# Kernel tuning notes

Measured on AMD Instinct MI355X. Metric: run time of the kernel, lower is better.

The kernel has to match this reference:

```python
import jax, jax.numpy as jnp
from jax import lax
import numpy as np

B, L, V, E, F, K, Y = 8, 2048, 51919, 100, 256, 9, 8921
PAD = K // 2  # 4, so conv output length == L


def setup_inputs() -> dict:
    key = jax.random.key(0)
    ks = jax.random.split(key, 8)
    return {
        "x": jax.random.randint(ks[0], (B, L), 0, 51917, dtype=jnp.int32),
        "target": jax.random.uniform(ks[1], (B, Y), dtype=jnp.float32),
        "embed_W": jax.random.normal(ks[2], (V, E), dtype=jnp.float32) * 0.1,
        "conv_w": jax.random.normal(ks[3], (F, E, K), dtype=jnp.float32) * (1.0 / np.sqrt(E * K)),
        "conv_b": jax.random.normal(ks[4], (F,), dtype=jnp.float32) * 0.01,
        "U_w": jax.random.normal(ks[5], (Y, F), dtype=jnp.float32) * (1.0 / np.sqrt(F)),
        "final_w": jax.random.normal(ks[6], (Y, F), dtype=jnp.float32) * (1.0 / np.sqrt(F)),
        "final_b": jax.random.normal(ks[7], (Y,), dtype=jnp.float32) * 0.01,
    }


def reference(x, target, embed_W, conv_w, conv_b, U_w, final_w, final_b):
    # Embedding lookup (dropout is identity at eval time)
    h = embed_W[x]                         # [B, L, E]
    h = jnp.transpose(h, (0, 2, 1))        # [B, E, L]
    # Conv1d, same-length padding
    h = lax.conv_general_dilated(
        h, conv_w, window_strides=(1,), padding=[(PAD, PAD)],
        dimension_numbers=("NCH", "OIH", "NCH"))
    h = jnp.tanh(h + conv_b[None, :, None])  # [B, F, L]
    h = jnp.transpose(h, (0, 2, 1))          # [B, L, F]
    # Per-label attention: scores [B, Y, L]
    scores = jnp.einsum("yf,blf->byl", U_w, h)
    alpha = jax.nn.softmax(scores, axis=2)   # [B, Y, L]
    m = jnp.einsum("byl,blf->byf", alpha, h)  # [B, Y, F]
    yhat = jnp.sum(final_w[None, :, :] * m, axis=2) + final_b  # [B, Y]
    # BCE with logits, mean reduction (stable form)
    loss = jnp.mean(jnp.maximum(yhat, 0.0) - yhat * target
                    + jnp.log1p(jnp.exp(-jnp.abs(yhat))))
    return yhat, loss, alpha
```

## Files before the change

kernel.cpp:

```cpp
#include <hip/hip_runtime.h>
#include <hip/hip_bf16.h>
#include <math.h>

#define B_ 8
#define L_ 2048
#define E_ 100
#define F_ 256
#define KW 9
#define Y_ 8921
#define YP 8960
#define KC 928
#define MC 16384

#define VMCNT(n) asm volatile("s_waitcnt vmcnt(" #n ")" ::: "memory")
#define CFENCE() asm volatile("" ::: "memory")

typedef __bf16 bf16x8 __attribute__((ext_vector_type(8)));
typedef float f32x4 __attribute__((ext_vector_type(4)));

__device__ __forceinline__ unsigned short f2bf(float v) {
  __hip_bfloat16 h = __float2bfloat16(v);
  return *reinterpret_cast<unsigned short*>(&h);
}

__device__ __forceinline__ void gld_lds16(const unsigned short* g, unsigned short* l) {
  __builtin_amdgcn_global_load_lds((const __attribute__((address_space(1))) void*)g,
                                   (__attribute__((address_space(3))) void*)l,
                                   16, 0, 0);
}

template <int STRIDE>
__device__ __forceinline__ void stage_tile(const unsigned short* __restrict__ g,
                                           unsigned short* __restrict__ lds, int tid) {
#pragma unroll
  for (int r = 0; r < 2; ++r) {
    int c = r * 256 + tid;
    gld_lds16(g + (size_t)(c >> 2) * STRIDE + (c & 3) * 8, lds + c * 8);
  }
}

__global__ __launch_bounds__(256) void im2col_kernel(const int* __restrict__ x,
                                                     const float* __restrict__ embedW,
                                                     unsigned short* __restrict__ im) {
  int idx = blockIdx.x * 256 + threadIdx.x;
  if (idx >= MC * (KC / 4)) return;
  int row = idx / (KC / 4), g4 = idx - row * (KC / 4);
  int kk = g4 * 4;
  ushort4 o = {0, 0, 0, 0};
  if (kk < 900) {
    int k = kk / 100, e = kk - k * 100;
    int b = row >> 11, l = row & 2047;
    int ls = l + k - 4;
    if (ls >= 0 && ls < L_) {
      const float4 v = *reinterpret_cast<const float4*>(
          &embedW[(size_t)x[b * L_ + ls] * E_ + e]);
      o.x = f2bf(v.x); o.y = f2bf(v.y); o.z = f2bf(v.z); o.w = f2bf(v.w);
    }
  }
  *reinterpret_cast<ushort4*>(&im[(size_t)idx * 4]) = o;
}

__global__ __launch_bounds__(256) void wpack_kernel(const float* __restrict__ convw,
                                                    unsigned short* __restrict__ wc) {
  int idx = blockIdx.x * 256 + threadIdx.x;
  if (idx >= F_ * KC) return;
  int f = idx / KC, kk = idx - f * KC;
  float v = 0.f;
  if (kk < 900) {
    int k = kk / 100, e = kk - k * 100;
    v = convw[f * 900 + e * 9 + k];
  }
  wc[idx] = f2bf(v);
}

__global__ __launch_bounds__(256) void ufpack_kernel(const float* __restrict__ Uw,
                                                     const float* __restrict__ Fww,
                                                     unsigned short* __restrict__ Ub,
                                                     unsigned short* __restrict__ Fwb) {
  int idx = blockIdx.x * 256 + threadIdx.x;
  if (idx >= 2 * YP * F_) return;
  int sel = idx / (YP * F_);
  int r = idx - sel * (YP * F_);
  int y = r / F_, f = r - y * F_;
  float v = (y < Y_) ? (sel ? Fww[y * F_ + f] : Uw[y * F_ + f]) : 0.f;
  (sel ? Fwb : Ub)[r] = f2bf(v);
}

__global__ __launch_bounds__(256) void conv_gemm(const unsigned short* __restrict__ A,
                                                 const unsigned short* __restrict__ Bt,
                                                 const float* __restrict__ convb,
                                                 unsigned short* __restrict__ hb) {
  __shared__ unsigned short As[3][128 * 32], Bs[3][128 * 32];
  const int mt = blockIdx.x, nt = blockIdx.y, tid = threadIdx.x;
  const unsigned short* Ag = A + (size_t)mt * 128 * KC;
  const unsigned short* Bg = Bt + (size_t)nt * 128 * KC;
  f32x4 acc[4][4] = {};
  const int lane = tid & 63, wv = tid >> 6;
  const int wy = wv >> 1, wx = wv & 1, lr = lane & 15, lq = lane >> 4;
  stage_tile<KC>(Ag, As[0], tid);
  stage_tile<KC>(Bg, Bs[0], tid);
  for (int kt = 0; kt < 29; ++kt) {
    const int cur = kt % 3;
    if (kt + 1 < 29) {
      const int nxt = (kt + 1) % 3;
      stage_tile<KC>(Ag + (kt + 1) * 32, As[nxt], tid);
      stage_tile<KC>(Bg + (kt + 1) * 32, Bs[nxt], tid);
      VMCNT(4);
    } else {
      VMCNT(0);
    }
    __builtin_amdgcn_s_barrier();
    CFENCE();
    bf16x8 a[4], bb[4];
#pragma unroll
    for (int i = 0; i < 4; ++i) a[i] = *(const bf16x8*)&As[cur][(wy * 64 + i * 16 + lr) * 32 + lq * 8];
#pragma unroll
    for (int j = 0; j < 4; ++j) bb[j] = *(const bf16x8*)&Bs[cur][(wx * 64 + j * 16 + lr) * 32 + lq * 8];
#pragma unroll
    for (int i = 0; i < 4; ++i)
#pragma unroll
      for (int j = 0; j < 4; ++j)
        acc[i][j] = __builtin_amdgcn_mfma_f32_16x16x32_bf16(a[i], bb[j], acc[i][j], 0, 0, 0);
  }
#pragma unroll
  for (int j = 0; j < 4; ++j) {
    const int n = nt * 128 + wx * 64 + j * 16 + lr;
    const float cb = convb[n];
#pragma unroll
    for (int i = 0; i < 4; ++i)
#pragma unroll
      for (int r = 0; r < 4; ++r) {
        const int m = mt * 128 + wy * 64 + i * 16 + lq * 4 + r;
        hb[(size_t)m * F_ + n] = f2bf(tanhf(acc[i][j][r] + cb));
      }
  }
}

__global__ __launch_bounds__(256) void scores_sum(const unsigned short* __restrict__ U,
                                                  const unsigned short* __restrict__ hb,
                                                  float* __restrict__ Spart) {
  __shared__ unsigned short As[3][128 * 32], Bs[3][128 * 32];
  __shared__ float rsum[128][2];
  const int yt = blockIdx.x, lt = blockIdx.y, b = blockIdx.z, tid = threadIdx.x;
  const unsigned short* Ag = U + (size_t)yt * 128 * F_;
  const unsigned short* Bg = hb + ((size_t)b * L_ + lt * 128) * F_;
  f32x4 acc[4][4] = {};
  const int lane = tid & 63, wv = tid >> 6;
  const int wy = wv >> 1, wx = wv & 1, lr = lane & 15, lq = lane >> 4;
  stage_tile<F_>(Ag, As[0], tid);
  stage_tile<F_>(Bg, Bs[0], tid);
  for (int kt = 0; kt < 8; ++kt) {
    const int cur = kt % 3;
    if (kt + 1 < 8) {
      const int nxt = (kt + 1) % 3;
      stage_tile<F_>(Ag + (kt + 1) * 32, As[nxt], tid);
      stage_tile<F_>(Bg + (kt + 1) * 32, Bs[nxt], tid);
      VMCNT(4);
    } else {
      VMCNT(0);
    }
    __builtin_amdgcn_s_barrier();
    CFENCE();
    bf16x8 a[4], bb[4];
#pragma unroll
    for (int i = 0; i < 4; ++i) a[i] = *(const bf16x8*)&As[cur][(wy * 64 + i * 16 + lr) * 32 + lq * 8];
#pragma unroll
    for (int j = 0; j < 4; ++j) bb[j] = *(const bf16x8*)&Bs[cur][(wx * 64 + j * 16 + lr) * 32 + lq * 8];
#pragma unroll
    for (int i = 0; i < 4; ++i)
#pragma unroll
      for (int j = 0; j < 4; ++j)
        acc[i][j] = __builtin_amdgcn_mfma_f32_16x16x32_bf16(a[i], bb[j], acc[i][j], 0, 0, 0);
  }
#pragma unroll
  for (int i = 0; i < 4; ++i)
#pragma unroll
    for (int r = 0; r < 4; ++r) {
      float rs = 0.f;
#pragma unroll
      for (int j = 0; j < 4; ++j) rs += __expf(acc[i][j][r]);
#pragma unroll
      for (int off = 1; off < 16; off <<= 1) rs += __shfl_xor(rs, off);
      if (lr == 0) rsum[wy * 64 + i * 16 + lq * 4 + r][wx] = rs;
    }
  __syncthreads();
  if (tid < 128)
    Spart[((size_t)b * YP + yt * 128 + tid) * 16 + lt] = rsum[tid][0] + rsum[tid][1];
}

__global__ __launch_bounds__(256) void sinv_kernel(const float* __restrict__ Spart,
                                                   float* __restrict__ Sinv) {
  int idx = blockIdx.x * 256 + threadIdx.x;
  if (idx >= B_ * YP) return;
  float s = 0.f;
#pragma unroll
  for (int t = 0; t < 16; ++t) s += Spart[(size_t)idx * 16 + t];
  Sinv[idx] = 1.f / s;
}

__global__ __launch_bounds__(256) void dual_gemm(const unsigned short* __restrict__ U,
                                                 const unsigned short* __restrict__ Fw,
                                                 const unsigned short* __restrict__ hb,
                                                 const float* __restrict__ Sinv,
                                                 float* __restrict__ alpha,
                                                 float* __restrict__ Npart) {
  __shared__ unsigned short As[3][128 * 32], As2[3][128 * 32], Bs[3][128 * 32];
  __shared__ float rsum[128][2];
  __shared__ float sinv[128];
  const int yt = blockIdx.x, lt = blockIdx.y, b = blockIdx.z, tid = threadIdx.x;
  if (tid < 128) sinv[tid] = Sinv[b * YP + yt * 128 + tid];
  __syncthreads();
  const unsigned short* Ag = U + (size_t)yt * 128 * F_;
  const unsigned short* Ag2 = Fw + (size_t)yt * 128 * F_;
  const unsigned short* Bg = hb + ((size_t)b * L_ + lt * 128) * F_;
  f32x4 accs[4][4] = {}, accg[4][4] = {};
  const int lane = tid & 63, wv = tid >> 6;
  const int wy = wv >> 1, wx = wv & 1, lr = lane & 15, lq = lane >> 4;
  stage_tile<F_>(Ag, As[0], tid);
  stage_tile<F_>(Ag2, As2[0], tid);
  stage_tile<F_>(Bg, Bs[0], tid);
  for (int kt = 0; kt < 8; ++kt) {
    const int cur = kt % 3;
    if (kt + 1 < 8) {
      const int nxt = (kt + 1) % 3;
      stage_tile<F_>(Ag + (kt + 1) * 32, As[nxt], tid);
      stage_tile<F_>(Ag2 + (kt + 1) * 32, As2[nxt], tid);
      stage_tile<F_>(Bg + (kt + 1) * 32, Bs[nxt], tid);
      VMCNT(6);
    } else {
      VMCNT(0);
    }
    __builtin_amdgcn_s_barrier();
    CFENCE();
    bf16x8 a1[4], a2[4], bb[4];
#pragma unroll
    for (int i = 0; i < 4; ++i) {
      a1[i] = *(const bf16x8*)&As[cur][(wy * 64 + i * 16 + lr) * 32 + lq * 8];
      a2[i] = *(const bf16x8*)&As2[cur][(wy * 64 + i * 16 + lr) * 32 + lq * 8];
    }
#pragma unroll
    for (int j = 0; j < 4; ++j) bb[j] = *(const bf16x8*)&Bs[cur][(wx * 64 + j * 16 + lr) * 32 + lq * 8];
#pragma unroll
    for (int i = 0; i < 4; ++i)
#pragma unroll
      for (int j = 0; j < 4; ++j) {
        accs[i][j] = __builtin_amdgcn_mfma_f32_16x16x32_bf16(a1[i], bb[j], accs[i][j], 0, 0, 0);
        accg[i][j] = __builtin_amdgcn_mfma_f32_16x16x32_bf16(a2[i], bb[j], accg[i][j], 0, 0, 0);
      }
  }
#pragma unroll
  for (int i = 0; i < 4; ++i)
#pragma unroll
    for (int r = 0; r < 4; ++r) {
      const int ml = wy * 64 + i * 16 + lq * 4 + r;
      const int y = yt * 128 + ml;
      const float si = sinv[ml];
      float ns = 0.f;
#pragma unroll
      for (int j = 0; j < 4; ++j) {
        const float av = __expf(accs[i][j][r]) * si;
        ns += av * accg[i][j][r];
        if (y < Y_) {
          const int l = lt * 128 + wx * 64 + j * 16 + lr;
          alpha[((size_t)b * Y_ + y) * L_ + l] = av;
        }
      }
#pragma unroll
      for (int off = 1; off < 16; off <<= 1) ns += __shfl_xor(ns, off);
      if (lr == 0) rsum[ml][wx] = ns;
    }
  __syncthreads();
  if (tid < 128)
    Npart[((size_t)b * YP + yt * 128 + tid) * 16 + lt] = rsum[tid][0] + rsum[tid][1];
}

__global__ __launch_bounds__(256) void yhat_loss_kernel(const float* __restrict__ Npart,
                                                        const float* __restrict__ Fb,
                                                        const float* __restrict__ target,
                                                        float* __restrict__ yhat,
                                                        float* __restrict__ part) {
  __shared__ float red[256];
  float s = 0.f;
  for (int i = blockIdx.x * 256 + threadIdx.x; i < B_ * Y_; i += gridDim.x * 256) {
    int b = i / Y_, y = i - b * Y_;
    float yh = Fb[y];
#pragma unroll
    for (int t = 0; t < 16; ++t) yh += Npart[((size_t)b * YP + y) * 16 + t];
    yhat[i] = yh;
    float tg = target[i];
    s += fmaxf(yh, 0.f) - yh * tg + log1pf(expf(-fabsf(yh)));
  }
  red[threadIdx.x] = s;
  __syncthreads();
  for (int o = 128; o > 0; o >>= 1) {
    if (threadIdx.x < o) red[threadIdx.x] += red[threadIdx.x + o];
    __syncthreads();
  }
  if (threadIdx.x == 0) part[blockIdx.x] = red[0];
}

__global__ __launch_bounds__(128) void loss_final_kernel(const float* __restrict__ part,
                                                         float* __restrict__ loss) {
  __shared__ float red[128];
  red[threadIdx.x] = part[threadIdx.x];
  __syncthreads();
  for (int o = 64; o > 0; o >>= 1) {
    if (threadIdx.x < o) red[threadIdx.x] += red[threadIdx.x + o];
    __syncthreads();
  }
  if (threadIdx.x == 0) loss[0] = red[0] * (1.f / (float)(B_ * Y_));
}

extern "C" void kernel_launch(void* const* d_in, const int* in_sizes, int n_in,
                              void* d_out, int out_size, void* d_ws, size_t ws_size,
                              hipStream_t stream) {
  const int* x = (const int*)d_in[0];
  const float* target = (const float*)d_in[1];
  const float* embedW = (const float*)d_in[2];
  const float* convw = (const float*)d_in[3];
  const float* convb = (const float*)d_in[4];
  const float* Uw = (const float*)d_in[5];
  const float* Fww = (const float*)d_in[6];
  const float* Fb = (const float*)d_in[7];

  float* out = (float*)d_out;
  float* yhat = out;
  float* loss = out + 71368;
  float* alpha = out + 71369;

  char* w = (char*)d_ws;
  size_t off = 0;
  auto alloc = [&](size_t bytes) -> void* {
    void* p = w + off;
    off += (bytes + 255) & ~(size_t)255;
    return p;
  };
  unsigned short* im2col = (unsigned short*)alloc((size_t)MC * KC * 2);
  unsigned short* wconv = (unsigned short*)alloc((size_t)F_ * KC * 2);
  unsigned short* Ub = (unsigned short*)alloc((size_t)YP * F_ * 2);
  unsigned short* Fwb = (unsigned short*)alloc((size_t)YP * F_ * 2);
  unsigned short* hb = (unsigned short*)alloc((size_t)MC * F_ * 2);
  float* Spart = (float*)alloc((size_t)B_ * YP * 16 * 4);
  float* Sinv = (float*)alloc((size_t)B_ * YP * 4);
  float* Npart = (float*)alloc((size_t)B_ * YP * 16 * 4);
  float* lpart = (float*)alloc(128 * 4);

  im2col_kernel<<<(MC * (KC / 4) + 255) / 256, 256, 0, stream>>>(x, embedW, im2col);
  wpack_kernel<<<(F_ * KC + 255) / 256, 256, 0, stream>>>(convw, wconv);
  ufpack_kernel<<<(2 * YP * F_ + 255) / 256, 256, 0, stream>>>(Uw, Fww, Ub, Fwb);
  conv_gemm<<<dim3(128, 2), 256, 0, stream>>>(im2col, wconv, convb, hb);
  scores_sum<<<dim3(70, 16, 8), 256, 0, stream>>>(Ub, hb, Spart);
  sinv_kernel<<<(B_ * YP + 255) / 256, 256, 0, stream>>>(Spart, Sinv);
  dual_gemm<<<dim3(70, 16, 8), 256, 0, stream>>>(Ub, Fwb, hb, Sinv, alpha, Npart);
  yhat_loss_kernel<<<128, 256, 0, stream>>>(Npart, Fb, target, yhat, lpart);
  loss_final_kernel<<<1, 128, 0, stream>>>(lpart, loss);
}
```

Measured before the change: 1.002 ms.

## Fuse attention score, softmax, and weighted sum into one persistent per-label-tile kernel

Replaces the scores_sum, sinv, dual_gemm and yhat reduction kernels with a single attn_fused kernel. Each block keeps a 128-label tile of U and final_w resident in LDS and loops over the full sequence twice: once to accumulate softmax denominators, once to write alpha and accumulate the yhat dot product. It also adds an XOR swizzle to LDS staging in conv_gemm to reduce bank conflicts. This removes the partial-sum buffers and extra launches, but the grid shrinks to 560 blocks of 512 threads with large LDS per block, which lowers parallelism and occupancy.

```diff
diff --git a/kernel.cpp b/kernel.cpp
--- a/kernel.cpp
+++ b/kernel.cpp
@@ -29,13 +29,14 @@
                                    16, 0, 0);
 }
 
-template <int STRIDE>
+template <int STRIDE, int NT>
 __device__ __forceinline__ void stage_tile(const unsigned short* __restrict__ g,
                                            unsigned short* __restrict__ lds, int tid) {
 #pragma unroll
-  for (int r = 0; r < 2; ++r) {
-    int c = r * 256 + tid;
-    gld_lds16(g + (size_t)(c >> 2) * STRIDE + (c & 3) * 8, lds + c * 8);
+  for (int r = 0; r < 512 / NT; ++r) {
+    int c = r * NT + tid;
+    int row = c >> 2, s = c & 3;
+    gld_lds16(g + (size_t)row * STRIDE + ((s ^ ((row >> 1) & 3)) * 8), lds + c * 8);
   }
 }
 
@@ -97,14 +98,15 @@
   f32x4 acc[4][4] = {};
   const int lane = tid & 63, wv = tid >> 6;
   const int wy = wv >> 1, wx = wv & 1, lr = lane & 15, lq = lane >> 4;
-  stage_tile<KC>(Ag, As[0], tid);
-  stage_tile<KC>(Bg, Bs[0], tid);
+  const int bOff = (lq ^ ((lr >> 1) & 3)) * 8;
+  stage_tile<KC, 256>(Ag, As[0], tid);
+  stage_tile<KC, 256>(Bg, Bs[0], tid);
   for (int kt = 0; kt < 29; ++kt) {
     const int cur = kt % 3;
     if (kt + 1 < 29) {
       const int nxt = (kt + 1) % 3;
-      stage_tile<KC>(Ag + (kt + 1) * 32, As[nxt], tid);
-      stage_tile<KC>(Bg + (kt + 1) * 32, Bs[nxt], tid);
+      stage_tile<KC, 256>(Ag + (kt + 1) * 32, As[nxt], tid);
+      stage_tile<KC, 256>(Bg + (kt + 1) * 32, Bs[nxt], tid);
       VMCNT(4);
     } else {
       VMCNT(0);
@@ -113,9 +115,9 @@
     CFENCE();
     bf16x8 a[4], bb[4];
 #pragma unroll
-    for (int i = 0; i < 4; ++i) a[i] = *(const bf16x8*)&As[cur][(wy * 64 + i * 16 + lr) * 32 + lq * 8];
-#pragma unroll
-    for (int j = 0; j < 4; ++j) bb[j] = *(const bf16x8*)&Bs[cur][(wx * 64 + j * 16 + lr) * 32 + lq * 8];
+    for (int i = 0; i < 4; ++i) a[i] = *(const bf16x8*)&As[cur][(wy * 64 + i * 16 + lr) * 32 + bOff];
+#pragma unroll
+    for (int j = 0; j < 4; ++j) bb[j] = *(const bf16x8*)&Bs[cur][(wx * 64 + j * 16 + lr) * 32 + bOff];
 #pragma unroll
     for (int i = 0; i < 4; ++i)
 #pragma unroll
@@ -136,159 +138,206 @@
   }
 }
 
-__global__ __launch_bounds__(256) void scores_sum(const unsigned short* __restrict__ U,
-                                                  const unsigned short* __restrict__ hb,
-                                                  float* __restrict__ Spart) {
-  __shared__ unsigned short As[3][128 * 32], Bs[3][128 * 32];
-  __shared__ float rsum[128][2];
-  const int yt = blockIdx.x, lt = blockIdx.y, b = blockIdx.z, tid = threadIdx.x;
-  const unsigned short* Ag = U + (size_t)yt * 128 * F_;
-  const unsigned short* Bg = hb + ((size_t)b * L_ + lt * 128) * F_;
-  f32x4 acc[4][4] = {};
+__global__ __launch_bounds__(512, 1) void attn_fused(const unsigned short* __restrict__ U,
+                                                     const unsigned short* __restrict__ Fw,
+                                                     const unsigned short* __restrict__ hb,
+                                                     const float* __restrict__ Fb,
+                                                     float* __restrict__ alpha,
+                                                     float* __restrict__ yhat) {
+  __shared__ unsigned short Us[128 * 256];
+  __shared__ unsigned short Fws[128 * 256];
+  __shared__ unsigned short Bs[3][128 * 32];
+  const int yt = blockIdx.x, b = blockIdx.y, tid = threadIdx.x;
   const int lane = tid & 63, wv = tid >> 6;
-  const int wy = wv >> 1, wx = wv & 1, lr = lane & 15, lq = lane >> 4;
-  stage_tile<F_>(Ag, As[0], tid);
-  stage_tile<F_>(Bg, Bs[0], tid);
-  for (int kt = 0; kt < 8; ++kt) {
-    const int cur = kt % 3;
-    if (kt + 1 < 8) {
-      const int nxt = (kt + 1) % 3;
-      stage_tile<F_>(Ag + (kt + 1) * 32, As[nxt], tid);
-      stage_tile<F_>(Bg + (kt + 1) * 32, Bs[nxt], tid);
-      VMCNT(4);
+  const int wy = wv >> 2, wx = wv & 3, lr = lane & 15, lq = lane >> 4;
+  const unsigned short* Ug = U + (size_t)yt * 128 * F_;
+  const unsigned short* Fg = Fw + (size_t)yt * 128 * F_;
+  const unsigned short* Hg = hb + (size_t)b * L_ * F_;
+
+#pragma unroll
+  for (int r = 0; r < 8; ++r) {
+    int c = r * 512 + tid;
+    int row = c >> 5, s = c & 31;
+    gld_lds16(Ug + row * F_ + ((s ^ (row & 7)) * 8), Us + c * 8);
+  }
+  {
+    int c = tid, row = c >> 2, s = c & 3;
+    gld_lds16(Hg + (size_t)row * F_ + ((s ^ ((row >> 1) & 3)) * 8), Bs[0] + c * 8);
+  }
+  VMCNT(0);
+  __builtin_amdgcn_s_barrier();
+  CFENCE();
+
+  const int bOff = (lq ^ ((lr >> 1) & 3)) * 8;
+  const int lr7 = lr & 7;
+
+  float rsA[4][4] = {};
+  f32x4 acc[4][2];
+  for (int t = 0; t < 128; ++t) {
+    const int kt = t & 7;
+    if (t + 1 < 128) {
+      const int c = tid, row = c >> 2, s = c & 3;
+      const int lt1 = (t + 1) >> 3, kt1 = (t + 1) & 7;
+      gld_lds16(Hg + (size_t)(lt1 * 128 + row) * F_ + kt1 * 32 + ((s ^ ((row >> 1) & 3)) * 8),
+                Bs[(t + 1) % 3] + c * 8);
+      VMCNT(1);
     } else {
       VMCNT(0);
     }
     __builtin_amdgcn_s_barrier();
     CFENCE();
-    bf16x8 a[4], bb[4];
-#pragma unroll
-    for (int i = 0; i < 4; ++i) a[i] = *(const bf16x8*)&As[cur][(wy * 64 + i * 16 + lr) * 32 + lq * 8];
-#pragma unroll
-    for (int j = 0; j < 4; ++j) bb[j] = *(const bf16x8*)&Bs[cur][(wx * 64 + j * 16 + lr) * 32 + lq * 8];
+    if (kt == 0) {
+#pragma unroll
+      for (int i = 0; i < 4; ++i)
+#pragma unroll
+        for (int j = 0; j < 2; ++j) acc[i][j] = (f32x4){0.f, 0.f, 0.f, 0.f};
+    }
+    const unsigned short* bs = Bs[t % 3];
+    const int colOff = (((kt * 4 + lq) ^ lr7)) * 8;
+    bf16x8 a[4], bbf[2];
+#pragma unroll
+    for (int i = 0; i < 4; ++i) a[i] = *(const bf16x8*)&Us[(wy * 64 + i * 16 + lr) * 256 + colOff];
+#pragma unroll
+    for (int j = 0; j < 2; ++j) bbf[j] = *(const bf16x8*)&bs[(wx * 32 + j * 16 + lr) * 32 + bOff];
 #pragma unroll
     for (int i = 0; i < 4; ++i)
 #pragma unroll
-      for (int j = 0; j < 4; ++j)
-        acc[i][j] = __builtin_amdgcn_mfma_f32_16x16x32_bf16(a[i], bb[j], acc[i][j], 0, 0, 0);
-  }
+      for (int j = 0; j < 2; ++j)
+        acc[i][j] = __builtin_amdgcn_mfma_f32_16x16x32_bf16(a[i], bbf[j], acc[i][j], 0, 0, 0);
+    if (kt == 7) {
+#pragma unroll
+      for (int i = 0; i < 4; ++i)
+#pragma unroll
+        for (int r = 0; r < 4; ++r) {
+          float rs = __expf(acc[i][0][r]) + __expf(acc[i][1][r]);
+#pragma unroll
+          for (int off = 1; off < 16; off <<= 1) rs += __shfl_xor(rs, off);
+          rsA[i][r] += rs;
+        }
+    }
+  }
+
+#pragma unroll
+  for (int r = 0; r < 8; ++r) {
+    int c = r * 512 + tid;
+    int row = c >> 5, s = c & 31;
+    gld_lds16(Fg + row * F_ + ((s ^ (row & 7)) * 8), Fws + c * 8);
+  }
+  __syncthreads();
+  float* red = (float*)Bs;
 #pragma unroll
   for (int i = 0; i < 4; ++i)
 #pragma unroll
+    for (int r = 0; r < 4; ++r)
+      if (lr == 0) red[(wy * 64 + i * 16 + lq * 4 + r) * 4 + wx] = rsA[i][r];
+  __syncthreads();
+  float si[4][4];
+#pragma unroll
+  for (int i = 0; i < 4; ++i)
+#pragma unroll
     for (int r = 0; r < 4; ++r) {
-      float rs = 0.f;
-#pragma unroll
-      for (int j = 0; j < 4; ++j) rs += __expf(acc[i][j][r]);
-#pragma unroll
-      for (int off = 1; off < 16; off <<= 1) rs += __shfl_xor(rs, off);
-      if (lr == 0) rsum[wy * 64 + i * 16 + lq * 4 + r][wx] = rs;
-    }
-  __syncthreads();
-  if (tid < 128)
-    Spart[((size_t)b * YP + yt * 128 + tid) * 16 + lt] = rsum[tid][0] + rsum[tid][1];
-}
-
-__global__ __launch_bounds__(256) void sinv_kernel(const float* __restrict__ Spart,
-                                                   float* __restrict__ Sinv) {
-  int idx = blockIdx.x * 256 + threadIdx.x;
-  if (idx >= B_ * YP) return;
-  float s = 0.f;
-#pragma unroll
-  for (int t = 0; t < 16; ++t) s += Spart[(size_t)idx * 16 + t];
-  Sinv[idx] = 1.f / s;
-}
-
-__global__ __launch_bounds__(256) void dual_gemm(const unsigned short* __restrict__ U,
-                                                 const unsigned short* __restrict__ Fw,
-                                                 const unsigned short* __restrict__ hb,
-                                                 const float* __restrict__ Sinv,
-                                                 float* __restrict__ alpha,
-                                                 float* __restrict__ Npart) {
-  __shared__ unsigned short As[3][128 * 32], As2[3][128 * 32], Bs[3][128 * 32];
-  __shared__ float rsum[128][2];
-  __shared__ float sinv[128];
-  const int yt = blockIdx.x, lt = blockIdx.y, b = blockIdx.z, tid = threadIdx.x;
-  if (tid < 128) sinv[tid] = Sinv[b * YP + yt * 128 + tid];
-  __syncthreads();
-  const unsigned short* Ag = U + (size_t)yt * 128 * F_;
-  const unsigned short* Ag2 = Fw + (size_t)yt * 128 * F_;
-  const unsigned short* Bg = hb + ((size_t)b * L_ + lt * 128) * F_;
-  f32x4 accs[4][4] = {}, accg[4][4] = {};
-  const int lane = tid & 63, wv = tid >> 6;
-  const int wy = wv >> 1, wx = wv & 1, lr = lane & 15, lq = lane >> 4;
-  stage_tile<F_>(Ag, As[0], tid);
-  stage_tile<F_>(Ag2, As2[0], tid);
-  stage_tile<F_>(Bg, Bs[0], tid);
-  for (int kt = 0; kt < 8; ++kt) {
-    const int cur = kt % 3;
-    if (kt + 1 < 8) {
-      const int nxt = (kt + 1) % 3;
-      stage_tile<F_>(Ag + (kt + 1) * 32, As[nxt], tid);
-      stage_tile<F_>(Ag2 + (kt + 1) * 32, As2[nxt], tid);
-      stage_tile<F_>(Bg + (kt + 1) * 32, Bs[nxt], tid);
-      VMCNT(6);
+      const int row = wy * 64 + i * 16 + lq * 4 + r;
+      si[i][r] = 1.f / (red[row * 4] + red[row * 4 + 1] + red[row * 4 + 2] + red[row * 4 + 3]);
+    }
+  __syncthreads();
+
+  {
+    int c = tid, row = c >> 2, s = c & 3;
+    gld_lds16(Hg + (size_t)row * F_ + ((s ^ ((row >> 1) & 3)) * 8), Bs[0] + c * 8);
+  }
+  VMCNT(0);
+  __builtin_amdgcn_s_barrier();
+  CFENCE();
+  float nsA[4][4] = {};
+  f32x4 accs[4][2], accg[4][2];
+  for (int t = 0; t < 128; ++t) {
+    const int kt = t & 7, lt = t >> 3;
+    if (t + 1 < 128) {
+      const int c = tid, row = c >> 2, s = c & 3;
+      const int lt1 = (t + 1) >> 3, kt1 = (t + 1) & 7;
+      gld_lds16(Hg + (size_t)(lt1 * 128 + row) * F_ + kt1 * 32 + ((s ^ ((row >> 1) & 3)) * 8),
+                Bs[(t + 1) % 3] + c * 8);
+      VMCNT(1);
     } else {
       VMCNT(0);
     }
     __builtin_amdgcn_s_barrier();
     CFENCE();
-    bf16x8 a1[4], a2[4], bb[4];
+    if (kt == 0) {
+#pragma unroll
+      for (int i = 0; i < 4; ++i)
+#pragma unroll
+        for (int j = 0; j < 2; ++j) {
+          accs[i][j] = (f32x4){0.f, 0.f, 0.f, 0.f};
+          accg[i][j] = (f32x4){0.f, 0.f, 0.f, 0.f};
+        }
+    }
+    const unsigned short* bs = Bs[t % 3];
+    const int colOff = (((kt * 4 + lq) ^ lr7)) * 8;
+    bf16x8 a1[4], a2[4], bbf[2];
 #pragma unroll
     for (int i = 0; i < 4; ++i) {
-      a1[i] = *(const bf16x8*)&As[cur][(wy * 64 + i * 16 + lr) * 32 + lq * 8];
-      a2[i] = *(const bf16x8*)&As2[cur][(wy * 64 + i * 16 + lr) * 32 + lq * 8];
-    }
-#pragma unroll
-    for (int j = 0; j < 4; ++j) bb[j] = *(const bf16x8*)&Bs[cur][(wx * 64 + j * 16 + lr) * 32 + lq * 8];
+      a1[i] = *(const bf16x8*)&Us[(wy * 64 + i * 16 + lr) * 256 + colOff];
+      a2[i] = *(const bf16x8*)&Fws[(wy * 64 + i * 16 + lr) * 256 + colOff];
+    }
+#pragma unroll
+    for (int j = 0; j < 2; ++j) bbf[j] = *(const bf16x8*)&bs[(wx * 32 + j * 16 + lr) * 32 + bOff];
 #pragma unroll
     for (int i = 0; i < 4; ++i)
 #pragma unroll
-      for (int j = 0; j < 4; ++j) {
-        accs[i][j] = __builtin_amdgcn_mfma_f32_16x16x32_bf16(a1[i], bb[j], accs[i][j], 0, 0, 0);
-        accg[i][j] = __builtin_amdgcn_mfma_f32_16x16x32_bf16(a2[i], bb[j], accg[i][j], 0, 0, 0);
+      for (int j = 0; j < 2; ++j) {
+        accs[i][j] = __builtin_amdgcn_mfma_f32_16x16x32_bf16(a1[i], bbf[j], accs[i][j], 0, 0, 0);
+        accg[i][j] = __builtin_amdgcn_mfma_f32_16x16x32_bf16(a2[i], bbf[j], accg[i][j], 0, 0, 0);
       }
-  }
+    if (kt == 7) {
+#pragma unroll
+      for (int i = 0; i < 4; ++i)
+#pragma unroll
+        for (int r = 0; r < 4; ++r) {
+          const int row = wy * 64 + i * 16 + lq * 4 + r;
+          const int y = yt * 128 + row;
+          const float sv = si[i][r];
+          float ns = 0.f;
+#pragma unroll
+          for (int j = 0; j < 2; ++j) {
+            const float av = __expf(accs[i][j][r]) * sv;
+            ns += av * accg[i][j][r];
+            if (y < Y_) {
+              const int l = lt * 128 + wx * 32 + j * 16 + lr;
+              alpha[((size_t)b * Y_ + y) * L_ + l] = av;
+            }
+          }
+#pragma unroll
+          for (int off = 1; off < 16; off <<= 1) ns += __shfl_xor(ns, off);
+          nsA[i][r] += ns;
+        }
+    }
+  }
+  __syncthreads();
+  float* red2 = (float*)Bs;
 #pragma unroll
   for (int i = 0; i < 4; ++i)
 #pragma unroll
-    for (int r = 0; r < 4; ++r) {
-      const int ml = wy * 64 + i * 16 + lq * 4 + r;
-      const int y = yt * 128 + ml;
-      const float si = sinv[ml];
-      float ns = 0.f;
-#pragma unroll
-      for (int j = 0; j < 4; ++j) {
-        const float av = __expf(accs[i][j][r]) * si;
-        ns += av * accg[i][j][r];
-        if (y < Y_) {
-          const int l = lt * 128 + wx * 64 + j * 16 + lr;
-          alpha[((size_t)b * Y_ + y) * L_ + l] = av;
-        }
-      }
-#pragma unroll
-      for (int off = 1; off < 16; off <<= 1) ns += __shfl_xor(ns, off);
-      if (lr == 0) rsum[ml][wx] = ns;
-    }
-  __syncthreads();
-  if (tid < 128)
-    Npart[((size_t)b * YP + yt * 128 + tid) * 16 + lt] = rsum[tid][0] + rsum[tid][1];
-}
-
-__global__ __launch_bounds__(256) void yhat_loss_kernel(const float* __restrict__ Npart,
-                                                        const float* __restrict__ Fb,
+    for (int r = 0; r < 4; ++r)
+      if (lr == 0) red2[(wy * 64 + i * 16 + lq * 4 + r) * 4 + wx] = nsA[i][r];
+  __syncthreads();
+  if (tid < 128) {
+    const int y = yt * 128 + tid;
+    if (y < Y_) {
+      yhat[(size_t)b * Y_ + y] = Fb[y] + red2[tid * 4] + red2[tid * 4 + 1] +
+                                 red2[tid * 4 + 2] + red2[tid * 4 + 3];
+    }
+  }
+}
+
+__global__ __launch_bounds__(256) void loss_part_kernel(const float* __restrict__ yhat,
                                                         const float* __restrict__ target,
-                                                        float* __restrict__ yhat,
                                                         float* __restrict__ part) {
   __shared__ float red[256];
   float s = 0.f;
   for (int i = blockIdx.x * 256 + threadIdx.x; i < B_ * Y_; i += gridDim.x * 256) {
-    int b = i / Y_, y = i - b * Y_;
-    float yh = Fb[y];
-#pragma unroll
-    for (int t = 0; t < 16; ++t) yh += Npart[((size_t)b * YP + y) * 16 + t];
-    yhat[i] = yh;
-    float tg = target[i];
-    s += fmaxf(yh, 0.f) - yh * tg + log1pf(expf(-fabsf(yh)));
+    float yh = yhat[i], t = target[i];
+    s += fmaxf(yh, 0.f) - yh * t + log1pf(expf(-fabsf(yh)));
   }
   red[threadIdx.x] = s;
   __syncthreads();
@@ -340,18 +389,13 @@
   unsigned short* Ub = (unsigned short*)alloc((size_t)YP * F_ * 2);
   unsigned short* Fwb = (unsigned short*)alloc((size_t)YP * F_ * 2);
   unsigned short* hb = (unsigned short*)alloc((size_t)MC * F_ * 2);
-  float* Spart = (float*)alloc((size_t)B_ * YP * 16 * 4);
-  float* Sinv = (float*)alloc((size_t)B_ * YP * 4);
-  float* Npart = (float*)alloc((size_t)B_ * YP * 16 * 4);
   float* lpart = (float*)alloc(128 * 4);
 
   im2col_kernel<<<(MC * (KC / 4) + 255) / 256, 256, 0, stream>>>(x, embedW, im2col);
   wpack_kernel<<<(F_ * KC + 255) / 256, 256, 0, stream>>>(convw, wconv);
   ufpack_kernel<<<(2 * YP * F_ + 255) / 256, 256, 0, stream>>>(Uw, Fww, Ub, Fwb);
   conv_gemm<<<dim3(128, 2), 256, 0, stream>>>(im2col, wconv, convb, hb);
-  scores_sum<<<dim3(70, 16, 8), 256, 0, stream>>>(Ub, hb, Spart);
-  sinv_kernel<<<(B_ * YP + 255) / 256, 256, 0, stream>>>(Spart, Sinv);
-  dual_gemm<<<dim3(70, 16, 8), 256, 0, stream>>>(Ub, Fwb, hb, Sinv, alpha, Npart);
-  yhat_loss_kernel<<<128, 256, 0, stream>>>(Npart, Fb, target, yhat, lpart);
+  attn_fused<<<dim3(70, 8), 512, 0, stream>>>(Ub, Fwb, hb, Fb, alpha, yhat);
+  loss_part_kernel<<<128, 256, 0, stream>>>(yhat, target, lpart);
   loss_final_kernel<<<1, 128, 0, stream>>>(lpart, loss);
 }
```

New measurement: 1.194 ms. 1.19x slower.

## Hold label weights in registers, swizzle LDS, and loop over L tiles in attention GEMMs

Applied to the files above, without the earlier changes.

Repacks U and final_w into an MFMA-fragment-friendly layout so each wave loads its A operands straight into registers once and keeps them there. The scores and dual GEMM kernels then iterate over several L tiles per block, streaming only h through LDS. Staging now uses an XOR-swizzled LDS layout in all GEMMs to cut bank conflicts. Npart partials drop from 16 to 8 per label. This removes repeated A-tile staging and the LDS traffic for A, at the cost of much higher register pressure (64 or 32 bf16x8 fragments per thread) and fewer blocks per launch.

```diff
diff --git a/kernel.cpp b/kernel.cpp
--- a/kernel.cpp
+++ b/kernel.cpp
@@ -6,13 +6,13 @@
 #define L_ 2048
 #define E_ 100
 #define F_ 256
-#define KW 9
 #define Y_ 8921
 #define YP 8960
 #define KC 928
 #define MC 16384
 
 #define VMCNT(n) asm volatile("s_waitcnt vmcnt(" #n ")" ::: "memory")
+#define LGKM0() asm volatile("s_waitcnt lgkmcnt(0)" ::: "memory")
 #define CFENCE() asm volatile("" ::: "memory")
 
 typedef __bf16 bf16x8 __attribute__((ext_vector_type(8)));
@@ -29,13 +29,14 @@
                                    16, 0, 0);
 }
 
-template <int STRIDE>
+template <int STRIDE, int NT>
 __device__ __forceinline__ void stage_tile(const unsigned short* __restrict__ g,
                                            unsigned short* __restrict__ lds, int tid) {
 #pragma unroll
-  for (int r = 0; r < 2; ++r) {
-    int c = r * 256 + tid;
-    gld_lds16(g + (size_t)(c >> 2) * STRIDE + (c & 3) * 8, lds + c * 8);
+  for (int r = 0; r < 512 / NT; ++r) {
+    int c = r * NT + tid;
+    int row = c >> 2, s = c & 3;
+    gld_lds16(g + (size_t)row * STRIDE + ((s ^ ((row >> 1) & 3)) * 8), lds + c * 8);
   }
 }
 
@@ -75,15 +76,19 @@
 
 __global__ __launch_bounds__(256) void ufpack_kernel(const float* __restrict__ Uw,
                                                      const float* __restrict__ Fww,
-                                                     unsigned short* __restrict__ Ub,
-                                                     unsigned short* __restrict__ Fwb) {
+                                                     unsigned short* __restrict__ U2,
+                                                     unsigned short* __restrict__ F2) {
   int idx = blockIdx.x * 256 + threadIdx.x;
   if (idx >= 2 * YP * F_) return;
   int sel = idx / (YP * F_);
   int r = idx - sel * (YP * F_);
-  int y = r / F_, f = r - y * F_;
+  int e = r & 7, t1 = r >> 3;
+  int yy = t1 & 127, t2 = t1 >> 7;
+  int lq = t2 & 3, t3 = t2 >> 2;
+  int kt = t3 & 7, yt = t3 >> 3;
+  int y = yt * 128 + yy, f = kt * 32 + lq * 8 + e;
   float v = (y < Y_) ? (sel ? Fww[y * F_ + f] : Uw[y * F_ + f]) : 0.f;
-  (sel ? Fwb : Ub)[r] = f2bf(v);
+  (sel ? F2 : U2)[r] = f2bf(v);
 }
 
 __global__ __launch_bounds__(256) void conv_gemm(const unsigned short* __restrict__ A,
@@ -97,14 +102,15 @@
   f32x4 acc[4][4] = {};
   const int lane = tid & 63, wv = tid >> 6;
   const int wy = wv >> 1, wx = wv & 1, lr = lane & 15, lq = lane >> 4;
-  stage_tile<KC>(Ag, As[0], tid);
-  stage_tile<KC>(Bg, Bs[0], tid);
+  const int bOff = (lq ^ ((lr >> 1) & 3)) * 8;
+  stage_tile<KC, 256>(Ag, As[0], tid);
+  stage_tile<KC, 256>(Bg, Bs[0], tid);
   for (int kt = 0; kt < 29; ++kt) {
     const int cur = kt % 3;
     if (kt + 1 < 29) {
       const int nxt = (kt + 1) % 3;
-      stage_tile<KC>(Ag + (kt + 1) * 32, As[nxt], tid);
-      stage_tile<KC>(Bg + (kt + 1) * 32, Bs[nxt], tid);
+      stage_tile<KC, 256>(Ag + (kt + 1) * 32, As[nxt], tid);
+      stage_tile<KC, 256>(Bg + (kt + 1) * 32, Bs[nxt], tid);
       VMCNT(4);
     } else {
       VMCNT(0);
@@ -113,9 +119,9 @@
     CFENCE();
     bf16x8 a[4], bb[4];
 #pragma unroll
-    for (int i = 0; i < 4; ++i) a[i] = *(const bf16x8*)&As[cur][(wy * 64 + i * 16 + lr) * 32 + lq * 8];
-#pragma unroll
-    for (int j = 0; j < 4; ++j) bb[j] = *(const bf16x8*)&Bs[cur][(wx * 64 + j * 16 + lr) * 32 + lq * 8];
+    for (int i = 0; i < 4; ++i) a[i] = *(const bf16x8*)&As[cur][(wy * 64 + i * 16 + lr) * 32 + bOff];
+#pragma unroll
+    for (int j = 0; j < 4; ++j) bb[j] = *(const bf16x8*)&Bs[cur][(wx * 64 + j * 16 + lr) * 32 + bOff];
 #pragma unroll
     for (int i = 0; i < 4; ++i)
 #pragma unroll
@@ -136,56 +142,78 @@
   }
 }
 
-__global__ __launch_bounds__(256) void scores_sum(const unsigned short* __restrict__ U,
-                                                  const unsigned short* __restrict__ hb,
-                                                  float* __restrict__ Spart) {
-  __shared__ unsigned short As[3][128 * 32], Bs[3][128 * 32];
+__global__ __launch_bounds__(256, 2) void scores_v3(const unsigned short* __restrict__ U2,
+                                                    const unsigned short* __restrict__ hb,
+                                                    float* __restrict__ Spart) {
+  __shared__ unsigned short Bs[3][128 * 32];
   __shared__ float rsum[128][2];
-  const int yt = blockIdx.x, lt = blockIdx.y, b = blockIdx.z, tid = threadIdx.x;
-  const unsigned short* Ag = U + (size_t)yt * 128 * F_;
-  const unsigned short* Bg = hb + ((size_t)b * L_ + lt * 128) * F_;
-  f32x4 acc[4][4] = {};
+  const int yt = blockIdx.x, lt2 = blockIdx.y, b = blockIdx.z, tid = threadIdx.x;
   const int lane = tid & 63, wv = tid >> 6;
   const int wy = wv >> 1, wx = wv & 1, lr = lane & 15, lq = lane >> 4;
-  stage_tile<F_>(Ag, As[0], tid);
-  stage_tile<F_>(Bg, Bs[0], tid);
-  for (int kt = 0; kt < 8; ++kt) {
-    const int cur = kt % 3;
-    if (kt + 1 < 8) {
-      const int nxt = (kt + 1) % 3;
-      stage_tile<F_>(Ag + (kt + 1) * 32, As[nxt], tid);
-      stage_tile<F_>(Bg + (kt + 1) * 32, Bs[nxt], tid);
-      VMCNT(4);
+  bf16x8 A[4][8];
+  {
+    const unsigned short* Up = U2 + (size_t)yt * (8 * 4 * 128 * 8);
+#pragma unroll
+    for (int i = 0; i < 4; ++i) {
+      const int yy = wy * 64 + i * 16 + lr;
+#pragma unroll
+      for (int kt = 0; kt < 8; ++kt)
+        A[i][kt] = *(const bf16x8*)&Up[((kt * 4 + lq) * 128 + yy) * 8];
+    }
+  }
+  const unsigned short* Hg = hb + ((size_t)b * L_ + (size_t)lt2 * 256) * F_;
+  const int bOff = (lq ^ ((lr >> 1) & 3)) * 8;
+  stage_tile<F_, 256>(Hg, Bs[0], tid);
+  f32x4 acc[4][4];
+  for (int t = 0; t < 16; ++t) {
+    const int kt = t & 7;
+    if (t + 1 < 16) {
+      stage_tile<F_, 256>(Hg + (size_t)((t + 1) >> 3) * 128 * F_ + ((t + 1) & 7) * 32,
+                          Bs[(t + 1) % 3], tid);
+      VMCNT(2);
     } else {
       VMCNT(0);
     }
     __builtin_amdgcn_s_barrier();
     CFENCE();
-    bf16x8 a[4], bb[4];
-#pragma unroll
-    for (int i = 0; i < 4; ++i) a[i] = *(const bf16x8*)&As[cur][(wy * 64 + i * 16 + lr) * 32 + lq * 8];
-#pragma unroll
-    for (int j = 0; j < 4; ++j) bb[j] = *(const bf16x8*)&Bs[cur][(wx * 64 + j * 16 + lr) * 32 + lq * 8];
+    if (kt == 0) {
+#pragma unroll
+      for (int i = 0; i < 4; ++i)
+#pragma unroll
+        for (int j = 0; j < 4; ++j) acc[i][j] = (f32x4){0.f, 0.f, 0.f, 0.f};
+    }
+    if (t == 8) {
+      if (tid < 128)
+        Spart[((size_t)b * YP + yt * 128 + tid) * 16 + lt2 * 2 + 0] =
+            rsum[tid][0] + rsum[tid][1];
+    }
+    const unsigned short* bs = Bs[t % 3];
+    bf16x8 bb[4];
+#pragma unroll
+    for (int j = 0; j < 4; ++j) bb[j] = *(const bf16x8*)&bs[(wx * 64 + j * 16 + lr) * 32 + bOff];
 #pragma unroll
     for (int i = 0; i < 4; ++i)
 #pragma unroll
       for (int j = 0; j < 4; ++j)
-        acc[i][j] = __builtin_amdgcn_mfma_f32_16x16x32_bf16(a[i], bb[j], acc[i][j], 0, 0, 0);
-  }
-#pragma unroll
-  for (int i = 0; i < 4; ++i)
-#pragma unroll
-    for (int r = 0; r < 4; ++r) {
-      float rs = 0.f;
-#pragma unroll
-      for (int j = 0; j < 4; ++j) rs += __expf(acc[i][j][r]);
-#pragma unroll
-      for (int off = 1; off < 16; off <<= 1) rs += __shfl_xor(rs, off);
-      if (lr == 0) rsum[wy * 64 + i * 16 + lq * 4 + r][wx] = rs;
-    }
+        acc[i][j] = __builtin_amdgcn_mfma_f32_16x16x32_bf16(A[i][kt], bb[j], acc[i][j], 0, 0, 0);
+    if (kt == 7) {
+#pragma unroll
+      for (int i = 0; i < 4; ++i)
+#pragma unroll
+        for (int r = 0; r < 4; ++r) {
+          float rs = 0.f;
+#pragma unroll
+          for (int j = 0; j < 4; ++j) rs += __expf(acc[i][j][r]);
+#pragma unroll
+          for (int off = 1; off < 16; off <<= 1) rs += __shfl_xor(rs, off);
+          if (lr == 0) rsum[wy * 64 + i * 16 + lq * 4 + r][wx] = rs;
+        }
+      LGKM0();
+    }
+  }
   __syncthreads();
   if (tid < 128)
-    Spart[((size_t)b * YP + yt * 128 + tid) * 16 + lt] = rsum[tid][0] + rsum[tid][1];
+    Spart[((size_t)b * YP + yt * 128 + tid) * 16 + lt2 * 2 + 1] = rsum[tid][0] + rsum[tid][1];
 }
 
 __global__ __launch_bounds__(256) void sinv_kernel(const float* __restrict__ Spart,
@@ -198,80 +226,108 @@
   Sinv[idx] = 1.f / s;
 }
 
-__global__ __launch_bounds__(256) void dual_gemm(const unsigned short* __restrict__ U,
-                                                 const unsigned short* __restrict__ Fw,
-                                                 const unsigned short* __restrict__ hb,
-                                                 const float* __restrict__ Sinv,
-                                                 float* __restrict__ alpha,
-                                                 float* __restrict__ Npart) {
-  __shared__ unsigned short As[3][128 * 32], As2[3][128 * 32], Bs[3][128 * 32];
-  __shared__ float rsum[128][2];
-  __shared__ float sinv[128];
-  const int yt = blockIdx.x, lt = blockIdx.y, b = blockIdx.z, tid = threadIdx.x;
-  if (tid < 128) sinv[tid] = Sinv[b * YP + yt * 128 + tid];
-  __syncthreads();
-  const unsigned short* Ag = U + (size_t)yt * 128 * F_;
-  const unsigned short* Ag2 = Fw + (size_t)yt * 128 * F_;
-  const unsigned short* Bg = hb + ((size_t)b * L_ + lt * 128) * F_;
-  f32x4 accs[4][4] = {}, accg[4][4] = {};
+__global__ __launch_bounds__(256, 2) void dual_v3(const unsigned short* __restrict__ U2,
+                                                  const unsigned short* __restrict__ F2,
+                                                  const unsigned short* __restrict__ hb,
+                                                  const float* __restrict__ Sinv,
+                                                  float* __restrict__ alpha,
+                                                  float* __restrict__ Npart) {
+  __shared__ unsigned short Bs[3][64 * 32];
+  const int yt = blockIdx.x, b = blockIdx.y, lz = blockIdx.z, tid = threadIdx.x;
   const int lane = tid & 63, wv = tid >> 6;
-  const int wy = wv >> 1, wx = wv & 1, lr = lane & 15, lq = lane >> 4;
-  stage_tile<F_>(Ag, As[0], tid);
-  stage_tile<F_>(Ag2, As2[0], tid);
-  stage_tile<F_>(Bg, Bs[0], tid);
-  for (int kt = 0; kt < 8; ++kt) {
-    const int cur = kt % 3;
-    if (kt + 1 < 8) {
-      const int nxt = (kt + 1) % 3;
-      stage_tile<F_>(Ag + (kt + 1) * 32, As[nxt], tid);
-      stage_tile<F_>(Ag2 + (kt + 1) * 32, As2[nxt], tid);
-      stage_tile<F_>(Bg + (kt + 1) * 32, Bs[nxt], tid);
-      VMCNT(6);
+  const int lr = lane & 15, lq = lane >> 4;
+  bf16x8 Au[2][8], Af[2][8];
+  {
+    const unsigned short* Up = U2 + (size_t)yt * (8 * 4 * 128 * 8);
+    const unsigned short* Fp = F2 + (size_t)yt * (8 * 4 * 128 * 8);
+#pragma unroll
+    for (int i = 0; i < 2; ++i) {
+      const int yy = wv * 32 + i * 16 + lr;
+#pragma unroll
+      for (int kt = 0; kt < 8; ++kt) {
+        Au[i][kt] = *(const bf16x8*)&Up[((kt * 4 + lq) * 128 + yy) * 8];
+        Af[i][kt] = *(const bf16x8*)&Fp[((kt * 4 + lq) * 128 + yy) * 8];
+      }
+    }
+  }
+  float si[2][4];
+#pragma unroll
+  for (int i = 0; i < 2; ++i)
+#pragma unroll
+    for (int r = 0; r < 4; ++r)
+      si[i][r] = Sinv[(size_t)b * YP + yt * 128 + wv * 32 + i * 16 + lq * 4 + r];
+  const unsigned short* Hg = hb + ((size_t)b * L_ + (size_t)lz * 256) * F_;
+  const int bOff = (lq ^ ((lr >> 1) & 3)) * 8;
+  {
+    int c = tid, row = c >> 2, s = c & 3;
+    gld_lds16(Hg + (size_t)row * F_ + ((s ^ ((row >> 1) & 3)) * 8), Bs[0] + c * 8);
+  }
+  float nsA[2][4] = {};
+  f32x4 accs[2][4], accg[2][4];
+  for (int t = 0; t < 32; ++t) {
+    const int kt = t & 7, l64 = t >> 3;
+    if (t + 1 < 32) {
+      int c = tid, row = c >> 2, s = c & 3;
+      gld_lds16(Hg + (size_t)(((t + 1) >> 3) * 64 + row) * F_ + ((t + 1) & 7) * 32 +
+                    ((s ^ ((row >> 1) & 3)) * 8),
+                Bs[(t + 1) % 3] + c * 8);
+      VMCNT(1);
     } else {
       VMCNT(0);
     }
     __builtin_amdgcn_s_barrier();
     CFENCE();
-    bf16x8 a1[4], a2[4], bb[4];
-#pragma unroll
-    for (int i = 0; i < 4; ++i) {
-      a1[i] = *(const bf16x8*)&As[cur][(wy * 64 + i * 16 + lr) * 32 + lq * 8];
-      a2[i] = *(const bf16x8*)&As2[cur][(wy * 64 + i * 16 + lr) * 32 + lq * 8];
-    }
-#pragma unroll
-    for (int j = 0; j < 4; ++j) bb[j] = *(const bf16x8*)&Bs[cur][(wx * 64 + j * 16 + lr) * 32 + lq * 8];
-#pragma unroll
-    for (int i = 0; i < 4; ++i)
+    if (kt == 0) {
+#pragma unroll
+      for (int i = 0; i < 2; ++i)
+#pragma unroll
+        for (int j = 0; j < 4; ++j) {
+          accs[i][j] = (f32x4){0.f, 0.f, 0.f, 0.f};
+          accg[i][j] = (f32x4){0.f, 0.f, 0.f, 0.f};
+        }
+    }
+    const unsigned short* bs = Bs[t % 3];
+    bf16x8 bb[4];
+#pragma unroll
+    for (int j = 0; j < 4; ++j) bb[j] = *(const bf16x8*)&bs[(j * 16 + lr) * 32 + bOff];
+#pragma unroll
+    for (int i = 0; i < 2; ++i)
 #pragma unroll
       for (int j = 0; j < 4; ++j) {
-        accs[i][j] = __builtin_amdgcn_mfma_f32_16x16x32_bf16(a1[i], bb[j], accs[i][j], 0, 0, 0);
-        accg[i][j] = __builtin_amdgcn_mfma_f32_16x16x32_bf16(a2[i], bb[j], accg[i][j], 0, 0, 0);
+        accs[i][j] = __builtin_amdgcn_mfma_f32_16x16x32_bf16(Au[i][kt], bb[j], accs[i][j], 0, 0, 0);
+        accg[i][j] = __builtin_amdgcn_mfma_f32_16x16x32_bf16(Af[i][kt], bb[j], accg[i][j], 0, 0, 0);
       }
-  }
-#pragma unroll
-  for (int i = 0; i < 4; ++i)
-#pragma unroll
-    for (int r = 0; r < 4; ++r) {
-      const int ml = wy * 64 + i * 16 + lq * 4 + r;
-      const int y = yt * 128 + ml;
-      const float si = sinv[ml];
-      float ns = 0.f;
-#pragma unroll
-      for (int j = 0; j < 4; ++j) {
-        const float av = __expf(accs[i][j][r]) * si;
-        ns += av * accg[i][j][r];
-        if (y < Y_) {
-          const int l = lt * 128 + wx * 64 + j * 16 + lr;
-          alpha[((size_t)b * Y_ + y) * L_ + l] = av;
+    if (kt == 7) {
+      const int lbase = lz * 256 + l64 * 64;
+#pragma unroll
+      for (int i = 0; i < 2; ++i) {
+        const int y0 = yt * 128 + wv * 32 + i * 16 + lq * 4;
+#pragma unroll
+        for (int r = 0; r < 4; ++r) {
+          float ns = 0.f;
+          const float sv = si[i][r];
+#pragma unroll
+          for (int j = 0; j < 4; ++j) {
+            const float av = __expf(accs[i][j][r]) * sv;
+            ns += av * accg[i][j][r];
+            if (y0 + r < Y_)
+              alpha[((size_t)b * Y_ + (y0 + r)) * L_ + lbase + j * 16 + lr] = av;
+          }
+#pragma unroll
+          for (int off = 1; off < 16; off <<= 1) ns += __shfl_xor(ns, off);
+          nsA[i][r] += ns;
         }
       }
-#pragma unroll
-      for (int off = 1; off < 16; off <<= 1) ns += __shfl_xor(ns, off);
-      if (lr == 0) rsum[ml][wx] = ns;
-    }
-  __syncthreads();
-  if (tid < 128)
-    Npart[((size_t)b * YP + yt * 128 + tid) * 16 + lt] = rsum[tid][0] + rsum[tid][1];
+    }
+  }
+#pragma unroll
+  for (int i = 0; i < 2; ++i)
+#pragma unroll
+    for (int r = 0; r < 4; ++r)
+      if (lr == 0) {
+        const int y = yt * 128 + wv * 32 + i * 16 + lq * 4 + r;
+        Npart[((size_t)b * YP + y) * 8 + lz] = nsA[i][r];
+      }
 }
 
 __global__ __launch_bounds__(256) void yhat_loss_kernel(const float* __restrict__ Npart,
@@ -285,7 +341,7 @@
     int b = i / Y_, y = i - b * Y_;
     float yh = Fb[y];
 #pragma unroll
-    for (int t = 0; t < 16; ++t) yh += Npart[((size_t)b * YP + y) * 16 + t];
+    for (int t = 0; t < 8; ++t) yh += Npart[((size_t)b * YP + y) * 8 + t];
     yhat[i] = yh;
     float tg = target[i];
     s += fmaxf(yh, 0.f) - yh * tg + log1pf(expf(-fabsf(yh)));
@@ -337,21 +393,21 @@
   };
   unsigned short* im2col = (unsigned short*)alloc((size_t)MC * KC * 2);
   unsigned short* wconv = (unsigned short*)alloc((size_t)F_ * KC * 2);
-  unsigned short* Ub = (unsigned short*)alloc((size_t)YP * F_ * 2);
-  unsigned short* Fwb = (unsigned short*)alloc((size_t)YP * F_ * 2);
+  unsigned short* U2 = (unsigned short*)alloc((size_t)YP * F_ * 2);
+  unsigned short* F2 = (unsigned short*)alloc((size_t)YP * F_ * 2);
   unsigned short* hb = (unsigned short*)alloc((size_t)MC * F_ * 2);
   float* Spart = (float*)alloc((size_t)B_ * YP * 16 * 4);
   float* Sinv = (float*)alloc((size_t)B_ * YP * 4);
-  float* Npart = (float*)alloc((size_t)B_ * YP * 16 * 4);
+  float* Npart = (float*)alloc((size_t)B_ * YP * 8 * 4);
   float* lpart = (float*)alloc(128 * 4);
 
   im2col_kernel<<<(MC * (KC / 4) + 255) / 256, 256, 0, stream>>>(x, embedW, im2col);
   wpack_kernel<<<(F_ * KC + 255) / 256, 256, 0, stream>>>(convw, wconv);
-  ufpack_kernel<<<(2 * YP * F_ + 255) / 256, 256, 0, stream>>>(Uw, Fww, Ub, Fwb);
+  ufpack_kernel<<<(2 * YP * F_ + 255) / 256, 256, 0, stream>>>(Uw, Fww, U2, F2);
   conv_gemm<<<dim3(128, 2), 256, 0, stream>>>(im2col, wconv, convb, hb);
-  scores_sum<<<dim3(70, 16, 8), 256, 0, stream>>>(Ub, hb, Spart);
+  scores_v3<<<dim3(70, 8, 8), 256, 0, stream>>>(U2, hb, Spart);
   sinv_kernel<<<(B_ * YP + 255) / 256, 256, 0, stream>>>(Spart, Sinv);
-  dual_gemm<<<dim3(70, 16, 8), 256, 0, stream>>>(Ub, Fwb, hb, Sinv, alpha, Npart);
+  dual_v3<<<dim3(70, 8, 8), 256, 0, stream>>>(U2, F2, hb, Sinv, alpha, Npart);
   yhat_loss_kernel<<<128, 256, 0, stream>>>(Npart, Fb, target, yhat, lpart);
   loss_final_kernel<<<1, 128, 0, stream>>>(lpart, loss);
 }
```

Result: slower. 1.584 ms (+58.1%).
